# Performance work log

Hardware: AMD Instinct MI355X
Metric: run time of the kernel (lower is better)

Reference implementation:

```python
import jax, jax.numpy as jnp
import numpy as np

NUM_CLASSES = 80  # COCO
BATCH = 32
CH = 3 * (5 + NUM_CLASSES)  # 255
THRESH = 0.6


def _decode_scale(out, anchors, t, thresh):
    """Dense YOLO decode for one scale.
    out: [B, 3*(5+C), H, W]; anchors: [3, 2]; t: stride.
    Returns boxes [B*H*W*3, 6] and valid mask [B*H*W*3].
    """
    B, Ch, H, W = out.shape
    v = jnp.transpose(out, (0, 2, 3, 1)).reshape(B, H, W, 3, -1)  # [B,H,W,3,5+C]
    conf = jax.nn.sigmoid(v[..., 0])
    valid = conf > thresh  # objectness mask (compaction mask in torch version)
    gx = jnp.arange(W, dtype=v.dtype)[None, None, :, None]  # idxs[:,2]
    gy = jnp.arange(H, dtype=v.dtype)[None, :, None, None]  # idxs[:,1]
    cx = (gx + jax.nn.sigmoid(v[..., 1])) * t
    cy = (gy + jax.nn.sigmoid(v[..., 2])) * t
    w = anchors[:, 0] * jnp.exp(v[..., 3])  # anchor dim broadcasts over [B,H,W,3]
    h = anchors[:, 1] * jnp.exp(v[..., 4])
    x1 = cx - w * 0.5
    y1 = cy - h * 0.5
    x2 = x1 + w
    y2 = y1 + h
    cls = jnp.argmax(v[..., 5:], axis=-1).astype(v.dtype)
    boxes = jnp.stack([conf, x1, y1, x2, y2, cls], axis=-1).reshape(-1, 6)
    return boxes, valid.reshape(-1)


def setup_inputs() -> dict:
    key = jax.random.key(0)
    k13, k26, k52 = jax.random.split(key, 3)
    output_13 = jax.random.normal(k13, (BATCH, CH, 13, 13), jnp.float32)
    output_26 = jax.random.normal(k26, (BATCH, CH, 26, 26), jnp.float32)
    output_52 = jax.random.normal(k52, (BATCH, CH, 52, 52), jnp.float32)
    # standard YOLOv3 COCO anchors per scale
    anchors_13 = jnp.array([[116., 90.], [156., 198.], [373., 326.]], jnp.float32)
    anchors_26 = jnp.array([[30., 61.], [62., 45.], [59., 119.]], jnp.float32)
    anchors_52 = jnp.array([[10., 13.], [16., 30.], [33., 23.]], jnp.float32)
    thresh = jnp.float32(THRESH)
    return {"output_13": output_13, "output_26": output_26, "output_52": output_52,
            "anchors_13": anchors_13, "anchors_26": anchors_26, "anchors_52": anchors_52,
            "thresh": thresh}


def reference(output_13, output_26, output_52, anchors_13, anchors_26, anchors_52, thresh):
    b13, m13 = _decode_scale(output_13, anchors_13, 32.0, thresh)
    b26, m26 = _decode_scale(output_26, anchors_26, 16.0, thresh)
    b52, m52 = _decode_scale(output_52, anchors_52, 8.0, thresh)
    boxes = jnp.concatenate([b13, b26, b52], axis=0)
    valid = jnp.concatenate([m13, m26, m52], axis=0)
    # boxes[valid] equals the torch module's concatenated output rows
    return boxes, valid
```

## Files before the change

kernel.cpp:

```cpp
#include <hip/hip_runtime.h>


constexpr int NCLS  = 80;
constexpr int BATCH = 32;
constexpr int HW13  = 169;
constexpr int HW26  = 676;
constexpr int HW52  = 2704;
constexpr int N13   = BATCH * 3 * HW13;
constexpr int N26   = BATCH * 3 * HW26;
constexpr int N52   = BATCH * 3 * HW52;
constexpr int NTOT  = N13 + N26 + N52;
constexpr int R13   = 0;
constexpr int R26   = N13;
constexpr int R52   = N13 + N26;

constexpr int OUT13 = (HW13 + 63) / 64;
constexpr int OUT26 = (HW26 / 4 + 63) / 64;
constexpr int OUT52 = (HW52 / 4 + 63) / 64;
constexpr int B13   = BATCH * OUT13;
constexpr int B26   = BATCH * OUT26;
constexpr int B52   = BATCH * OUT52;
constexpr int NBLK  = B13 + B26 + B52;

__device__ __forceinline__ float sigm(float x) { return 1.0f / (1.0f + expf(-x)); }

template <int HW, int W>
__device__ __forceinline__ void decode_scalar(
    const float* __restrict__ in, const float* __restrict__ anc,
    float t, int b, int a, int hw, int rowofs, float th,
    float* __restrict__ boxes, float* __restrict__ valid)
{
    const int x = hw % W;
    const int y = hw / W;
    const float* p = in + (size_t)(b * 255 + a * 85) * HW + hw;

    const float t0 = p[0];
    const float t1 = p[(size_t)1 * HW];
    const float t2 = p[(size_t)2 * HW];
    const float t3 = p[(size_t)3 * HW];
    const float t4 = p[(size_t)4 * HW];

    float best = p[(size_t)5 * HW];
    int cls = 0;
#pragma unroll
    for (int k = 1; k < NCLS; ++k) {
        const float v = p[(size_t)(5 + k) * HW];
        cls  = v > best ? k : cls;
        best = fmaxf(v, best);
    }

    const float aw = anc[a * 2 + 0], ah = anc[a * 2 + 1];
    const float conf = sigm(t0);
    const float cx   = ((float)x + sigm(t1)) * t;
    const float cy   = ((float)y + sigm(t2)) * t;
    const float w    = aw * expf(t3);
    const float h    = ah * expf(t4);
    const float x1   = cx - w * 0.5f;
    const float y1   = cy - h * 0.5f;

    const int row = rowofs + (b * HW + hw) * 3 + a;
    float* o = boxes + (size_t)row * 6;
    o[0] = conf; o[1] = x1; o[2] = y1; o[3] = x1 + w; o[4] = y1 + h; o[5] = (float)cls;
    valid[row] = conf > th ? 1.0f : 0.0f;
}

template <int HW, int W>
__device__ __forceinline__ void decode_vec4(
    const float* __restrict__ in, const float* __restrict__ anc,
    float t, int b, int a, int c, int rowofs, float th,
    float* __restrict__ boxes, float* __restrict__ valid)
{
    constexpr int HWc = HW / 4;
    const float4* __restrict__ p =
        reinterpret_cast<const float4*>(in + (size_t)(b * 255 + a * 85) * HW) + c;

    const float4 t0 = p[0];
    const float4 t1 = p[(size_t)1 * HWc];
    const float4 t2 = p[(size_t)2 * HWc];
    const float4 t3 = p[(size_t)3 * HWc];
    const float4 t4 = p[(size_t)4 * HWc];

    float4 bv = p[(size_t)5 * HWc];
    float b0 = bv.x, b1 = bv.y, b2 = bv.z, b3 = bv.w;
    int c0 = 0, c1 = 0, c2 = 0, c3 = 0;
#pragma unroll
    for (int k = 1; k < NCLS; ++k) {
        const float4 v = p[(size_t)(5 + k) * HWc];
        c0 = v.x > b0 ? k : c0;  b0 = fmaxf(v.x, b0);
        c1 = v.y > b1 ? k : c1;  b1 = fmaxf(v.y, b1);
        c2 = v.z > b2 ? k : c2;  b2 = fmaxf(v.z, b2);
        c3 = v.w > b3 ? k : c3;  b3 = fmaxf(v.w, b3);
    }

    const float aw = anc[a * 2 + 0], ah = anc[a * 2 + 1];

#define EMIT(j, s0, s1, s2, s3, s4, cc)                                   \
    {                                                                     \
        const int hw = 4 * c + (j);                                       \
        const int x = hw % W;                                             \
        const int y = hw / W;                                             \
        const float conf = sigm(s0);                                      \
        const float cx = ((float)x + sigm(s1)) * t;                       \
        const float cy = ((float)y + sigm(s2)) * t;                       \
        const float w_ = aw * expf(s3);                                   \
        const float h_ = ah * expf(s4);                                   \
        const float x1 = cx - w_ * 0.5f;                                  \
        const float y1 = cy - h_ * 0.5f;                                  \
        const int row = rowofs + (b * HW + hw) * 3 + a;                   \
        float* o = boxes + (size_t)row * 6;                               \
        o[0] = conf; o[1] = x1; o[2] = y1;                                \
        o[3] = x1 + w_; o[4] = y1 + h_; o[5] = (float)(cc);               \
        valid[row] = conf > th ? 1.0f : 0.0f;                             \
    }

    EMIT(0, t0.x, t1.x, t2.x, t3.x, t4.x, c0);
    EMIT(1, t0.y, t1.y, t2.y, t3.y, t4.y, c1);
    EMIT(2, t0.z, t1.z, t2.z, t3.z, t4.z, c2);
    EMIT(3, t0.w, t1.w, t2.w, t3.w, t4.w, c3);
#undef EMIT
}

__global__ __launch_bounds__(192) void yolo_decode_kernel(
    const float* __restrict__ in13, const float* __restrict__ in26,
    const float* __restrict__ in52,
    const float* __restrict__ a13, const float* __restrict__ a26,
    const float* __restrict__ a52,
    const float* __restrict__ pth, float* __restrict__ out)
{
    const int a    = threadIdx.x >> 6;
    const int lane = threadIdx.x & 63;
    const float th = *pth;
    float* boxes = out;
    float* valid = out + (size_t)NTOT * 6;

    int blk = blockIdx.x;
    if (blk < B13) {
        const int b  = blk / OUT13;
        const int co = blk % OUT13;
        const int hw = co * 64 + lane;
        if (hw >= HW13) return;
        decode_scalar<HW13, 13>(in13, a13, 32.0f, b, a, hw, R13, th, boxes, valid);
    } else if (blk < B13 + B26) {
        blk -= B13;
        const int b  = blk / OUT26;
        const int co = blk % OUT26;
        const int c  = co * 64 + lane;
        if (c >= HW26 / 4) return;
        decode_vec4<HW26, 26>(in26, a26, 16.0f, b, a, c, R26, th, boxes, valid);
    } else {
        blk -= (B13 + B26);
        const int b  = blk / OUT52;
        const int co = blk % OUT52;
        const int c  = co * 64 + lane;
        if (c >= HW52 / 4) return;
        decode_vec4<HW52, 52>(in52, a52, 8.0f, b, a, c, R52, th, boxes, valid);
    }
}

extern "C" void kernel_launch(void* const* d_in, const int* in_sizes, int n_in,
                              void* d_out, int out_size, void* d_ws, size_t ws_size,
                              hipStream_t stream) {
    const float* in13 = (const float*)d_in[0];
    const float* in26 = (const float*)d_in[1];
    const float* in52 = (const float*)d_in[2];
    const float* a13  = (const float*)d_in[3];
    const float* a26  = (const float*)d_in[4];
    const float* a52  = (const float*)d_in[5];
    const float* pth  = (const float*)d_in[6];
    float* out = (float*)d_out;

    yolo_decode_kernel<<<NBLK, 192, 0, stream>>>(in13, in26, in52,
                                                 a13, a26, a52, pth, out);
}
```

Before: 28.89 us.

## Split anchors into separate single-wave blocks and schedule largest scale first

Each 192-thread block, which held three anchor waves, becomes three 64-thread blocks. Block IDs are interleaved in groups of 24 so that sibling anchor blocks stay adjacent, and the 52x52 scale, which is the heaviest, is dispatched first. The goal is finer-grained scheduling across CUs and less tail imbalance. The cost is more blocks to launch and per-block overhead for the index decode.

```diff
diff --git a/kernel.cpp b/kernel.cpp
--- a/kernel.cpp
+++ b/kernel.cpp
@@ -14,13 +14,16 @@
 constexpr int R26   = N13;
 constexpr int R52   = N13 + N26;
 
-constexpr int OUT13 = (HW13 + 63) / 64;
-constexpr int OUT26 = (HW26 / 4 + 63) / 64;
-constexpr int OUT52 = (HW52 / 4 + 63) / 64;
-constexpr int B13   = BATCH * OUT13;
-constexpr int B26   = BATCH * OUT26;
-constexpr int B52   = BATCH * OUT52;
-constexpr int NBLK  = B13 + B26 + B52;
+constexpr int CO52 = 11;
+constexpr int CO26 = 3;
+constexpr int CO13 = 3;
+constexpr int S52  = BATCH * CO52;
+constexpr int S26  = BATCH * CO26;
+constexpr int S13  = BATCH * CO13;
+constexpr int NB52 = S52 * 3;
+constexpr int NB26 = S26 * 3;
+constexpr int NB13 = S13 * 3;
+constexpr int NBLK = NB52 + NB26 + NB13;
 
 __device__ __forceinline__ float sigm(float x) { return 1.0f / (1.0f + expf(-x)); }
 
@@ -120,40 +123,48 @@
 #undef EMIT
 }
 
-__global__ __launch_bounds__(192) void yolo_decode_kernel(
+__device__ __forceinline__ void sib_decode(int id, int& a, int& s)
+{
+    const int g   = id / 24;
+    const int rem = id % 24;
+    a = rem >> 3;
+    s = g * 8 + (rem & 7);
+}
+
+__global__ __launch_bounds__(64, 3) void yolo_decode_kernel(
     const float* __restrict__ in13, const float* __restrict__ in26,
     const float* __restrict__ in52,
     const float* __restrict__ a13, const float* __restrict__ a26,
     const float* __restrict__ a52,
     const float* __restrict__ pth, float* __restrict__ out)
 {
-    const int a    = threadIdx.x >> 6;
-    const int lane = threadIdx.x & 63;
+    const int lane = threadIdx.x;
     const float th = *pth;
     float* boxes = out;
     float* valid = out + (size_t)NTOT * 6;
 
-    int blk = blockIdx.x;
-    if (blk < B13) {
-        const int b  = blk / OUT13;
-        const int co = blk % OUT13;
-        const int hw = co * 64 + lane;
-        if (hw >= HW13) return;
-        decode_scalar<HW13, 13>(in13, a13, 32.0f, b, a, hw, R13, th, boxes, valid);
-    } else if (blk < B13 + B26) {
-        blk -= B13;
-        const int b  = blk / OUT26;
-        const int co = blk % OUT26;
+    int id = blockIdx.x;
+    if (id < NB52) {
+        int a, s;  sib_decode(id, a, s);
+        const int b  = s / CO52;
+        const int co = s % CO52;
+        const int c  = co * 64 + lane;
+        if (c >= HW52 / 4) return;
+        decode_vec4<HW52, 52>(in52, a52, 8.0f, b, a, c, R52, th, boxes, valid);
+    } else if (id < NB52 + NB26) {
+        int a, s;  sib_decode(id - NB52, a, s);
+        const int b  = s / CO26;
+        const int co = s % CO26;
         const int c  = co * 64 + lane;
         if (c >= HW26 / 4) return;
         decode_vec4<HW26, 26>(in26, a26, 16.0f, b, a, c, R26, th, boxes, valid);
     } else {
-        blk -= (B13 + B26);
-        const int b  = blk / OUT52;
-        const int co = blk % OUT52;
-        const int c  = co * 64 + lane;
-        if (c >= HW52 / 4) return;
-        decode_vec4<HW52, 52>(in52, a52, 8.0f, b, a, c, R52, th, boxes, valid);
+        int a, s;  sib_decode(id - NB52 - NB26, a, s);
+        const int b  = s / CO13;
+        const int co = s % CO13;
+        const int hw = co * 64 + lane;
+        if (hw >= HW13) return;
+        decode_scalar<HW13, 13>(in13, a13, 32.0f, b, a, hw, R13, th, boxes, valid);
     }
 }
 
@@ -169,6 +180,6 @@
     const float* pth  = (const float*)d_in[6];
     float* out = (float*)d_out;
 
-    yolo_decode_kernel<<<NBLK, 192, 0, stream>>>(in13, in26, in52,
-                                                 a13, a26, a52, pth, out);
+    yolo_decode_kernel<<<NBLK, 64, 0, stream>>>(in13, in26, in52,
+                                                a13, a26, a52, pth, out);
 }
```

New measurement: 40.37 us. 1.4x slower.
